# Optimization experiments

Measured on AMD Instinct MI355X. Metric: run time of the kernel, lower is better.

The kernel has to match this reference:

```python
import jax, jax.numpy as jnp
import numpy as np

B, C, Z, H, W = 1, 64, 8, 32, 32
C8 = C // 8


def setup_inputs() -> dict:
    key = jax.random.key(0)
    ks = jax.random.split(key, 8)
    shp = (B, C, Z, H, W)
    return {
        "x1": jax.random.normal(ks[0], shp, dtype=jnp.float32),
        "x2": jax.random.normal(ks[1], shp, dtype=jnp.float32),
        # 1x1x1 Conv3d weights are pointwise channel matmuls: [out, in]
        "Wf": jax.random.normal(ks[2], (C8, C), dtype=jnp.float32) * (1.0 / np.sqrt(C)),
        "bf": jnp.zeros((C8,), dtype=jnp.float32),
        "Wg": jax.random.normal(ks[3], (C8, C), dtype=jnp.float32) * (1.0 / np.sqrt(C)),
        "bg": jnp.zeros((C8,), dtype=jnp.float32),
        "Wh1": jax.random.normal(ks[4], (C, C), dtype=jnp.float32) * (1.0 / np.sqrt(C)),
        "bh1": jnp.zeros((C,), dtype=jnp.float32),
        "Wh2": jax.random.normal(ks[5], (C, C), dtype=jnp.float32) * (1.0 / np.sqrt(C)),
        "bh2": jnp.zeros((C,), dtype=jnp.float32),
        "gamma1": jax.random.uniform(ks[6], (1,), dtype=jnp.float32),
        "gamma2": jax.random.uniform(ks[7], (1,), dtype=jnp.float32),
    }


def _attend(x, Wf, bf, Wg, bg, Wh, bh, gamma):
    b, c, z, h, w = x.shape
    n = z * h * w
    xf = x.reshape(b, c, n)                                  # [B, C, N]
    f = jnp.einsum('oc,bcn->bno', Wf, xf) + bf               # [B, N, C//8]
    g = jnp.einsum('oc,bcn->bon', Wg, xf) + bg[:, None]      # [B, C//8, N]
    # unscaled attention logits, softmax over last dim (torch dim=2)
    att = jax.nn.softmax(jnp.einsum('bnk,bkm->bnm', f, g), axis=2)  # [B, N, N]
    v = jnp.einsum('oc,bcn->bon', Wh, xf) + bh[:, None]      # [B, C, N]
    sa = jnp.einsum('bcn,bnm->bcm', v, att).reshape(x.shape)  # h @ attention
    return gamma * sa + x


def reference(x1, x2, Wf, bf, Wg, bg, Wh1, bh1, Wh2, bh2, gamma1, gamma2):
    y1 = _attend(x1, Wf, bf, Wg, bg, Wh1, bh1, gamma1)
    y2 = _attend(x2, Wf, bf, Wg, bg, Wh2, bh2, gamma2)
    return (y1, y2)
```

## Files before the change

kernel.cpp:

```cpp
#include <hip/hip_runtime.h>
#include <math.h>

#define N 8192
#define WSP (80*N)
#define OFF_G (8*N)
#define OFF_T (16*N)

typedef __attribute__((ext_vector_type(8)))  short bf16x8;
typedef __attribute__((ext_vector_type(4)))  float f32x4;
typedef __attribute__((ext_vector_type(16))) float f32x16;

#define ZERO16 ((f32x16){0.f,0.f,0.f,0.f,0.f,0.f,0.f,0.f,0.f,0.f,0.f,0.f,0.f,0.f,0.f,0.f})

#if defined(__has_builtin)
#  if __has_builtin(__builtin_amdgcn_exp2f)
#    define EXP2(x) __builtin_amdgcn_exp2f(x)
#  endif
#endif
#ifndef EXP2
#  define EXP2(x) exp2f(x)
#endif

__device__ __forceinline__ unsigned short bf_hi(float x) {
    union { float f; unsigned u; } v; v.f = x;
    unsigned r = v.u + 0x7fffu + ((v.u >> 16) & 1u);
    return (unsigned short)(r >> 16);
}
__device__ __forceinline__ float bf_f(unsigned short h) {
    union { float f; unsigned u; } v; v.u = ((unsigned)h) << 16;
    return v.f;
}
__device__ __forceinline__ unsigned pack_hi16(unsigned i1, unsigned i0) {
#if defined(__has_builtin) && __has_builtin(__builtin_amdgcn_perm)
    return __builtin_amdgcn_perm(i1, i0, 0x07060302u);
#else
    return (i1 & 0xffff0000u) | (i0 >> 16);
#endif
}

__device__ __forceinline__ void xcd_map(int lin, int& a, int& idx) {
    int xcd = lin & 7;
    a   = xcd >> 2;
    idx = (xcd & 3) | ((lin >> 3) << 2);
}

__global__ __launch_bounds__(512) void prep_kernel(
    const float* __restrict__ x1, const float* __restrict__ x2,
    const float* __restrict__ Wf, const float* __restrict__ bf,
    const float* __restrict__ Wg, const float* __restrict__ bg,
    const float* __restrict__ Wh1, const float* __restrict__ bh1,
    const float* __restrict__ Wh2, const float* __restrict__ bh2,
    float* __restrict__ ws)
{
    int a, bidx;
    xcd_map(blockIdx.x + (int)gridDim.x * blockIdx.y, a, bidx);
    const float* x  = a ? x2  : x1;
    const float* Wh = a ? Wh2 : Wh1;
    const float* bh = a ? bh2 : bh1;
    float* base = ws + (size_t)a * WSP;
    unsigned short* F16 = (unsigned short*)base;
    unsigned short* G16 = (unsigned short*)(base + OFF_G);
    float* vb = base + OFF_T;

    __shared__ __align__(16) float xs[32][68];
    __shared__ __align__(16) float Wlds[80][64];
    __shared__ float blds[80];

    const int n0 = bidx * 32;
    const int t  = threadIdx.x;
    for (int i = t; i < 64*32; i += 512) {
        int c = i >> 5, j = i & 31;
        xs[j][c] = x[(size_t)c*N + n0 + j];
    }
    for (int i4 = t; i4 < 80*16; i4 += 512) {
        int o = i4 >> 4, c4 = i4 & 15;
        const float* src = (o < 8) ? (Wf + o*64) : (o < 16) ? (Wg + (o-8)*64) : (Wh + (o-16)*64);
        *(f32x4*)&Wlds[o][c4*4] = *(const f32x4*)(src + c4*4);
    }
    if (t < 80) blds[t] = (t < 8) ? bf[t] : (t < 16) ? bg[t-8] : bh[t-16];
    __syncthreads();

    const int j  = t & 31;
    const int og = t >> 5;
    float s[5];
    #pragma unroll
    for (int k = 0; k < 5; ++k) s[k] = blds[og + 16*k];
    const f32x4* xrow = (const f32x4*)&xs[j][0];
    #pragma unroll 4
    for (int c4 = 0; c4 < 16; ++c4) {
        const f32x4 xv = xrow[c4];
        #pragma unroll
        for (int k = 0; k < 5; ++k) {
            const f32x4 wv = *(const f32x4*)&Wlds[og + 16*k][c4*4];
            s[k] += wv.x * xv.x;
            s[k] += wv.y * xv.y;
            s[k] += wv.z * xv.z;
            s[k] += wv.w * xv.w;
        }
    }
    const float LOG2E = 1.44269504088896340736f;
    #pragma unroll
    for (int k = 0; k < 5; ++k) {
        int o = og + 16*k;
        if (o < 8) {
            float v = s[k] * LOG2E;
            unsigned short h = bf_hi(v);
            F16[(size_t)(n0+j)*16 + o]     = h;
            F16[(size_t)(n0+j)*16 + 8 + o] = bf_hi(v - bf_f(h));
        } else if (o < 16) {
            float v = s[k];
            unsigned short h = bf_hi(v);
            G16[(size_t)(n0+j)*16 + (o-8)]     = h;
            G16[(size_t)(n0+j)*16 + 8 + (o-8)] = bf_hi(v - bf_f(h));
        } else {
            vb[(size_t)(o-16)*N + n0 + j] = s[k];
        }
    }
}

__global__ __launch_bounds__(512, 4) void rownorm_kernel(float* __restrict__ ws)
{
    int a, bidx;
    xcd_map(blockIdx.x + (int)gridDim.x * blockIdx.y, a, bidx);
    float* base = ws + (size_t)a * WSP;
    const unsigned short* F16 = (const unsigned short*)base;
    const unsigned short* G16 = (const unsigned short*)(base + OFF_G);
    float* vb = base + OFF_T;
    const int n0 = bidx * 32;
    const int t  = threadIdx.x;
    const int w = t >> 6, lane = t & 63, l31 = lane & 31, hi = lane >> 5;

    __shared__ float vbs[32][65];
    __shared__ float lsum[8][32];
    __shared__ float linv[32];

    {
        const int c = t >> 3, g = t & 7;
        const f32x4 v = __builtin_nontemporal_load(
            (const f32x4*)(vb + (size_t)c*N + n0 + g*4));
        vbs[g*4+0][c] = v.x;
        vbs[g*4+1][c] = v.y;
        vbs[g*4+2][c] = v.z;
        vbs[g*4+3][c] = v.w;
    }

    const bf16x8 A1 = *(const bf16x8*)(F16 + (size_t)(n0 + l31)*16 + hi*8);
    const bf16x8 z8 = {0,0,0,0,0,0,0,0};
    const bf16x8 A2 = hi ? z8 : A1;

    const int mb = w * (N/8);
    const int MM = (N/8) - 1;
    bf16x8 B1, B2;
    f32x16 S, sum = ZERO16;

    B1 = *(const bf16x8*)(G16 + (size_t)(mb + l31)*16);
    B2 = *(const bf16x8*)(G16 + (size_t)(mb + l31)*16 + 8);
    S = __builtin_amdgcn_mfma_f32_32x32x16_bf16(A1, B1, ZERO16, 0, 0, 0);
    S = __builtin_amdgcn_mfma_f32_32x32x16_bf16(A2, B2, S, 0, 0, 0);
    B1 = *(const bf16x8*)(G16 + (size_t)(mb + 32 + l31)*16);
    B2 = *(const bf16x8*)(G16 + (size_t)(mb + 32 + l31)*16 + 8);

    for (int it = 0; it < 32; ++it) {
        f32x16 Sn = __builtin_amdgcn_mfma_f32_32x32x16_bf16(A1, B1, ZERO16, 0, 0, 0);
        Sn = __builtin_amdgcn_mfma_f32_32x32x16_bf16(A2, B2, Sn, 0, 0, 0);
        {
            const size_t mrow = mb + (((it+2)*32) & MM) + l31;
            B1 = *(const bf16x8*)(G16 + mrow*16);
            B2 = *(const bf16x8*)(G16 + mrow*16 + 8);
        }
        #pragma unroll
        for (int r = 0; r < 16; ++r)
            sum[r] += __uint_as_float(__float_as_uint(EXP2(S[r])) & 0xffff0000u);
        S = Sn;
    }
    #pragma unroll
    for (int r = 0; r < 16; ++r) {
        float v = sum[r];
        v += __shfl_xor(v, 1, 64);
        v += __shfl_xor(v, 2, 64);
        v += __shfl_xor(v, 4, 64);
        v += __shfl_xor(v, 8, 64);
        v += __shfl_xor(v, 16, 64);
        sum[r] = v;
    }
    if (l31 == 0) {
        #pragma unroll
        for (int r = 0; r < 16; ++r) {
            int n = (r & 3) + 8*(r >> 2) + 4*hi;
            lsum[w][n] = sum[r];
        }
    }
    __syncthreads();
    if (t < 32) {
        float v = 0.f;
        #pragma unroll
        for (int ww = 0; ww < 8; ++ww) v += lsum[ww][t];
        linv[t] = 1.0f / v;
    }
    __syncthreads();

    if (t < 256) {
        const int c = t >> 2, kkg = t & 3;
        bf16x8 H;
        #pragma unroll
        for (int jj = 0; jj < 8; ++jj) {
            int n_rd = (kkg >> 1)*16 + 4*(kkg & 1) + (jj & 3) + 8*((jj >> 2) & 1);
            H[jj] = (short)bf_hi(vbs[n_rd][c] * linv[n_rd]);
        }
        unsigned short* tile = (unsigned short*)(base + OFF_T) + (size_t)(n0 >> 5) * 4096;
        *(bf16x8*)(tile + c*32 + kkg*8) = H;
    }
}

__global__ __launch_bounds__(768, 3) void attn_kernel(
    const float* __restrict__ x1, const float* __restrict__ x2,
    const float* __restrict__ ga1, const float* __restrict__ ga2,
    const float* __restrict__ ws, float* __restrict__ out_)
{
    int a, bidx;
    xcd_map(blockIdx.x + (int)gridDim.x * blockIdx.y, a, bidx);
    const float* x = a ? x2 : x1;
    const float gamma = a ? ga2[0] : ga1[0];
    const float* base = ws + (size_t)a * WSP;
    const unsigned short* F16 = (const unsigned short*)base;
    const unsigned short* G16 = (const unsigned short*)(base + OFF_G);
    const unsigned short* tiles = (const unsigned short*)(base + OFF_T);
    float* out = out_ + (size_t)a * ((size_t)64 * N);

    const int m0 = bidx * 64;
    const int t = threadIdx.x;
    const int w = t >> 6, lane = t & 63, l31 = lane & 31, hi = lane >> 5;

    const bf16x8 z8 = {0,0,0,0,0,0,0,0};
    bf16x8 Bh0, Bl0, Bh1, Bl1;
    {
        const unsigned short* gp0 = G16 + (size_t)(m0 + l31)*16;
        const unsigned short* gp1 = G16 + (size_t)(m0 + 32 + l31)*16;
        Bh0 = *(const bf16x8*)gp0;
        Bl0 = hi ? z8 : *(const bf16x8*)(gp0 + 8);
        Bh1 = *(const bf16x8*)gp1;
        Bl1 = hi ? z8 : *(const bf16x8*)(gp1 + 8);
    }

    f32x16 accA = ZERO16, accB = ZERO16;
    f32x16 accC = ZERO16, accD = ZERO16;

    const int beg = 21*w + (w < 4 ? w : 4);
    const int end = beg + (w < 4 ? 22 : 21);

    bf16x8 Acur, Anxt;
    bf16x8 AH[4];

    Acur = *(const bf16x8*)(F16 + ((size_t)beg*32 + l31)*16 + hi*8);
    Anxt = *(const bf16x8*)(F16 + ((size_t)(beg+1)*32 + l31)*16 + hi*8);
    {
        const unsigned short* tb = tiles + (size_t)beg * 4096;
        #pragma unroll
        for (int kp = 0; kp < 2; ++kp)
            #pragma unroll
            for (int ct = 0; ct < 2; ++ct)
                AH[kp*2+ct] = *(const bf16x8*)(tb + (ct*32 + l31)*32 + kp*16 + hi*8);
    }

    for (int it = beg; it < end; ++it) {
        int in1 = it + 1; if (in1 >= end) in1 -= (end - beg);
        int in2 = it + 2; if (in2 >= end) in2 -= (end - beg);

        f32x16 S0 = __builtin_amdgcn_mfma_f32_32x32x16_bf16(Acur, Bh0, ZERO16, 0, 0, 0);
        f32x16 S1 = __builtin_amdgcn_mfma_f32_32x32x16_bf16(Acur, Bh1, ZERO16, 0, 0, 0);
        S0 = __builtin_amdgcn_mfma_f32_32x32x16_bf16(Acur, Bl0, S0, 0, 0, 0);
        S1 = __builtin_amdgcn_mfma_f32_32x32x16_bf16(Acur, Bl1, S1, 0, 0, 0);
        Acur = Anxt;
        Anxt = *(const bf16x8*)(F16 + ((size_t)in2*32 + l31)*16 + hi*8);

        union BU { bf16x8 v; unsigned u[4]; };
        BU pH0[2], pH1[2];
        #pragma unroll
        for (int kp = 0; kp < 2; ++kp)
            #pragma unroll
            for (int d = 0; d < 4; ++d) {
                float q0 = EXP2(S0[kp*8 + 2*d]);
                float q1 = EXP2(S0[kp*8 + 2*d + 1]);
                pH0[kp].u[d] = pack_hi16(__float_as_uint(q1), __float_as_uint(q0));
                float q2 = EXP2(S1[kp*8 + 2*d]);
                float q3 = EXP2(S1[kp*8 + 2*d + 1]);
                pH1[kp].u[d] = pack_hi16(__float_as_uint(q3), __float_as_uint(q2));
            }

        #pragma unroll
        for (int kp = 0; kp < 2; ++kp) {
            accA = __builtin_amdgcn_mfma_f32_32x32x16_bf16(AH[kp*2+0], pH0[kp].v, accA, 0, 0, 0);
            accC = __builtin_amdgcn_mfma_f32_32x32x16_bf16(AH[kp*2+0], pH1[kp].v, accC, 0, 0, 0);
            accB = __builtin_amdgcn_mfma_f32_32x32x16_bf16(AH[kp*2+1], pH0[kp].v, accB, 0, 0, 0);
            accD = __builtin_amdgcn_mfma_f32_32x32x16_bf16(AH[kp*2+1], pH1[kp].v, accD, 0, 0, 0);
        }

        {
            const unsigned short* tb = tiles + (size_t)in1 * 4096;
            #pragma unroll
            for (int kp = 0; kp < 2; ++kp)
                #pragma unroll
                for (int ct = 0; ct < 2; ++ct)
                    AH[kp*2+ct] = *(const bf16x8*)(tb + (ct*32 + l31)*32 + kp*16 + hi*8);
        }
    }

    __shared__ float red[64][65];
    for (int ww = 0; ww < 12; ++ww) {
        if (w == ww) {
            #pragma unroll
            for (int mg = 0; mg < 2; ++mg)
                #pragma unroll
                for (int ct = 0; ct < 2; ++ct) {
                    const f32x16& Ac = mg ? (ct ? accD : accC) : (ct ? accB : accA);
                    #pragma unroll
                    for (int r = 0; r < 16; ++r) {
                        int c = ct*32 + (r & 3) + 8*(r >> 2) + 4*hi;
                        int m = mg*32 + l31;
                        if (ww == 0) red[c][m]  = Ac[r];
                        else         red[c][m] += Ac[r];
                    }
                }
        }
        __syncthreads();
    }
    for (int e = t; e < 64*64; e += 768) {
        int c = e >> 6, m = e & 63;
        size_t gi = (size_t)c*N + m0 + m;
        float xv = __builtin_nontemporal_load(x + gi);
        __builtin_nontemporal_store(gamma * red[c][m] + xv, out + gi);
    }
}

extern "C" void kernel_launch(void* const* d_in, const int* in_sizes, int n_in,
                              void* d_out, int out_size, void* d_ws, size_t ws_size,
                              hipStream_t stream)
{
    (void)in_sizes; (void)n_in; (void)out_size; (void)ws_size;
    const float* x1  = (const float*)d_in[0];
    const float* x2  = (const float*)d_in[1];
    const float* Wf  = (const float*)d_in[2];
    const float* bf  = (const float*)d_in[3];
    const float* Wg  = (const float*)d_in[4];
    const float* bg  = (const float*)d_in[5];
    const float* Wh1 = (const float*)d_in[6];
    const float* bh1 = (const float*)d_in[7];
    const float* Wh2 = (const float*)d_in[8];
    const float* bh2 = (const float*)d_in[9];
    const float* g1  = (const float*)d_in[10];
    const float* g2  = (const float*)d_in[11];
    float* out = (float*)d_out;
    float* ws  = (float*)d_ws;

    prep_kernel   <<<dim3(N/32, 2), dim3(512), 0, stream>>>(x1,x2,Wf,bf,Wg,bg,Wh1,bh1,Wh2,bh2,ws);
    rownorm_kernel<<<dim3(N/32, 2), dim3(512), 0, stream>>>(ws);
    attn_kernel   <<<dim3(N/64, 2), dim3(768), 0, stream>>>(x1,x2,g1,g2,ws,out);
}
```

Measured before the change: 141.4 us.

## Software-pipeline logits MFMA one iteration ahead of exp and PV MFMAs

Restructures the inner attention loop so the logit MFMAs for the next tile are issued while exp2 and pack run on the current tile. The PV MFMAs are split into two halves interleaved with the exp work. The aim is to hide MFMA latency behind VALU transcendental work instead of stalling on S0/S1 each iteration. It adds a prologue and keeps S0/S1 live across iterations, which raises register pressure.

Result: no change. 139.5 us (-1.3%).

```diff
diff --git a/kernel.cpp b/kernel.cpp
--- a/kernel.cpp
+++ b/kernel.cpp
@@ -248,11 +248,18 @@
     const int beg = 21*w + (w < 4 ? w : 4);
     const int end = beg + (w < 4 ? 22 : 21);
 
-    bf16x8 Acur, Anxt;
+    bf16x8 Acur;
     bf16x8 AH[4];
-
-    Acur = *(const bf16x8*)(F16 + ((size_t)beg*32 + l31)*16 + hi*8);
-    Anxt = *(const bf16x8*)(F16 + ((size_t)(beg+1)*32 + l31)*16 + hi*8);
+    f32x16 S0, S1;
+
+    {
+        const bf16x8 A0 = *(const bf16x8*)(F16 + ((size_t)beg*32 + l31)*16 + hi*8);
+        S0 = __builtin_amdgcn_mfma_f32_32x32x16_bf16(A0, Bh0, ZERO16, 0, 0, 0);
+        S1 = __builtin_amdgcn_mfma_f32_32x32x16_bf16(A0, Bh1, ZERO16, 0, 0, 0);
+        S0 = __builtin_amdgcn_mfma_f32_32x32x16_bf16(A0, Bl0, S0, 0, 0, 0);
+        S1 = __builtin_amdgcn_mfma_f32_32x32x16_bf16(A0, Bl1, S1, 0, 0, 0);
+    }
+    Acur = *(const bf16x8*)(F16 + ((size_t)(beg+1)*32 + l31)*16 + hi*8);
     {
         const unsigned short* tb = tiles + (size_t)beg * 4096;
         #pragma unroll
@@ -262,38 +269,48 @@
                 AH[kp*2+ct] = *(const bf16x8*)(tb + (ct*32 + l31)*32 + kp*16 + hi*8);
     }
 
+    union BU { bf16x8 v; unsigned u[4]; };
+
     for (int it = beg; it < end; ++it) {
         int in1 = it + 1; if (in1 >= end) in1 -= (end - beg);
         int in2 = it + 2; if (in2 >= end) in2 -= (end - beg);
 
-        f32x16 S0 = __builtin_amdgcn_mfma_f32_32x32x16_bf16(Acur, Bh0, ZERO16, 0, 0, 0);
-        f32x16 S1 = __builtin_amdgcn_mfma_f32_32x32x16_bf16(Acur, Bh1, ZERO16, 0, 0, 0);
+        BU pH0a, pH1a;
+        #pragma unroll
+        for (int d = 0; d < 4; ++d) {
+            float q0 = EXP2(S0[2*d]);
+            float q1 = EXP2(S0[2*d + 1]);
+            pH0a.u[d] = pack_hi16(__float_as_uint(q1), __float_as_uint(q0));
+            float q2 = EXP2(S1[2*d]);
+            float q3 = EXP2(S1[2*d + 1]);
+            pH1a.u[d] = pack_hi16(__float_as_uint(q3), __float_as_uint(q2));
+        }
+        accA = __builtin_amdgcn_mfma_f32_32x32x16_bf16(AH[0], pH0a.v, accA, 0, 0, 0);
+        accC = __builtin_amdgcn_mfma_f32_32x32x16_bf16(AH[0], pH1a.v, accC, 0, 0, 0);
+        accB = __builtin_amdgcn_mfma_f32_32x32x16_bf16(AH[1], pH0a.v, accB, 0, 0, 0);
+        accD = __builtin_amdgcn_mfma_f32_32x32x16_bf16(AH[1], pH1a.v, accD, 0, 0, 0);
+
+        BU pH0b, pH1b;
+        #pragma unroll
+        for (int d = 0; d < 4; ++d) {
+            float q0 = EXP2(S0[8 + 2*d]);
+            float q1 = EXP2(S0[8 + 2*d + 1]);
+            pH0b.u[d] = pack_hi16(__float_as_uint(q1), __float_as_uint(q0));
+            float q2 = EXP2(S1[8 + 2*d]);
+            float q3 = EXP2(S1[8 + 2*d + 1]);
+            pH1b.u[d] = pack_hi16(__float_as_uint(q3), __float_as_uint(q2));
+        }
+
+        S0 = __builtin_amdgcn_mfma_f32_32x32x16_bf16(Acur, Bh0, ZERO16, 0, 0, 0);
+        S1 = __builtin_amdgcn_mfma_f32_32x32x16_bf16(Acur, Bh1, ZERO16, 0, 0, 0);
         S0 = __builtin_amdgcn_mfma_f32_32x32x16_bf16(Acur, Bl0, S0, 0, 0, 0);
         S1 = __builtin_amdgcn_mfma_f32_32x32x16_bf16(Acur, Bl1, S1, 0, 0, 0);
-        Acur = Anxt;
-        Anxt = *(const bf16x8*)(F16 + ((size_t)in2*32 + l31)*16 + hi*8);
-
-        union BU { bf16x8 v; unsigned u[4]; };
-        BU pH0[2], pH1[2];
-        #pragma unroll
-        for (int kp = 0; kp < 2; ++kp)
-            #pragma unroll
-            for (int d = 0; d < 4; ++d) {
-                float q0 = EXP2(S0[kp*8 + 2*d]);
-                float q1 = EXP2(S0[kp*8 + 2*d + 1]);
-                pH0[kp].u[d] = pack_hi16(__float_as_uint(q1), __float_as_uint(q0));
-                float q2 = EXP2(S1[kp*8 + 2*d]);
-                float q3 = EXP2(S1[kp*8 + 2*d + 1]);
-                pH1[kp].u[d] = pack_hi16(__float_as_uint(q3), __float_as_uint(q2));
-            }
-
-        #pragma unroll
-        for (int kp = 0; kp < 2; ++kp) {
-            accA = __builtin_amdgcn_mfma_f32_32x32x16_bf16(AH[kp*2+0], pH0[kp].v, accA, 0, 0, 0);
-            accC = __builtin_amdgcn_mfma_f32_32x32x16_bf16(AH[kp*2+0], pH1[kp].v, accC, 0, 0, 0);
-            accB = __builtin_amdgcn_mfma_f32_32x32x16_bf16(AH[kp*2+1], pH0[kp].v, accB, 0, 0, 0);
-            accD = __builtin_amdgcn_mfma_f32_32x32x16_bf16(AH[kp*2+1], pH1[kp].v, accD, 0, 0, 0);
-        }
+        Acur = *(const bf16x8*)(F16 + ((size_t)in2*32 + l31)*16 + hi*8);
+
+        accA = __builtin_amdgcn_mfma_f32_32x32x16_bf16(AH[2], pH0b.v, accA, 0, 0, 0);
+        accC = __builtin_amdgcn_mfma_f32_32x32x16_bf16(AH[2], pH1b.v, accC, 0, 0, 0);
+        accB = __builtin_amdgcn_mfma_f32_32x32x16_bf16(AH[3], pH0b.v, accB, 0, 0, 0);
+        accD = __builtin_amdgcn_mfma_f32_32x32x16_bf16(AH[3], pH1b.v, accD, 0, 0, 0);
 
         {
             const unsigned short* tb = tiles + (size_t)in1 * 4096;
```

## Use 8 waves with 32 tiles each and a two-stage software pipeline

Applied to the files above, without the earlier changes.

The attention kernel drops from 12 to 8 wavefronts per block, and each wave now owns exactly 32 key tiles instead of an uneven 21/22 split. The main loop is restructured to handle two tiles per iteration: the logits MFMAs for the next pair are issued after the PV MFMAs of the current pair, and tile and A-operand loads are prefetched one stage ahead. This aims to hide exp/pack latency and memory latency behind MFMA work and to shorten the cross-wave shared-memory reduction. In exchange it raises register pressure and gives fewer waves per CU (launch bounds 512,2), which can reduce latency hiding.

Measured after the change: 148.2 us. 4.9% more time.

```diff
diff --git a/kernel.cpp b/kernel.cpp
--- a/kernel.cpp
+++ b/kernel.cpp
@@ -212,7 +212,50 @@
     }
 }
 
-__global__ __launch_bounds__(768, 3) void attn_kernel(
+#define MFMA_(A_, B_, C_) __builtin_amdgcn_mfma_f32_32x32x16_bf16(A_, B_, C_, 0, 0, 0)
+
+#define PACK_QUAD(P0_, P1_, S0_, S1_, O_)                                      \
+    _Pragma("unroll")                                                          \
+    for (int d = 0; d < 4; ++d) {                                              \
+        float q0 = EXP2(S0_[(O_) + 2*d]), q1 = EXP2(S0_[(O_) + 2*d + 1]);      \
+        P0_.u[d] = pack_hi16(__float_as_uint(q1), __float_as_uint(q0));        \
+        float q2 = EXP2(S1_[(O_) + 2*d]), q3 = EXP2(S1_[(O_) + 2*d + 1]);      \
+        P1_.u[d] = pack_hi16(__float_as_uint(q3), __float_as_uint(q2));        \
+    }
+
+#define CHUNK_PV(S0_, S1_, T0_, T1_, T2_, T3_)                                 \
+    {                                                                          \
+        BU u0_, u1_;                                                           \
+        PACK_QUAD(u0_, u1_, S0_, S1_, 0)                                       \
+        accA = MFMA_(T0_, u0_.v, accA);                                        \
+        accC = MFMA_(T0_, u1_.v, accC);                                        \
+        accB = MFMA_(T1_, u0_.v, accB);                                        \
+        accD = MFMA_(T1_, u1_.v, accD);                                        \
+        BU v0_, v1_;                                                           \
+        PACK_QUAD(v0_, v1_, S0_, S1_, 8)                                       \
+        accA = MFMA_(T2_, v0_.v, accA);                                        \
+        accC = MFMA_(T2_, v1_.v, accC);                                        \
+        accB = MFMA_(T3_, v0_.v, accB);                                        \
+        accD = MFMA_(T3_, v1_.v, accD);                                        \
+    }
+
+#define LOAD_TILES(T0_, T1_, T2_, T3_, REL_)                                   \
+    {                                                                          \
+        const unsigned short* tb_ = tiles + (size_t)(cb + ((REL_) & 31)) * 4096; \
+        T0_ = *(const bf16x8*)(tb_ + (0*32 + l31)*32 + 0*16 + hi*8);           \
+        T1_ = *(const bf16x8*)(tb_ + (1*32 + l31)*32 + 0*16 + hi*8);           \
+        T2_ = *(const bf16x8*)(tb_ + (0*32 + l31)*32 + 1*16 + hi*8);           \
+        T3_ = *(const bf16x8*)(tb_ + (1*32 + l31)*32 + 1*16 + hi*8);           \
+    }
+
+#define LOAD_A(DST_, REL_)                                                     \
+    DST_ = *(const bf16x8*)(F16 + (size_t)((cb + ((REL_) & 31))*32 + l31)*16 + hi*8);
+
+#define LOGITS(S0_, S1_, A_)                                                   \
+    S0_ = MFMA_(A_, Bh0, ZERO16); S1_ = MFMA_(A_, Bh1, ZERO16);                \
+    S0_ = MFMA_(A_, Bl0, S0_);    S1_ = MFMA_(A_, Bl1, S1_);
+
+__global__ __launch_bounds__(512, 2) void attn_kernel(
     const float* __restrict__ x1, const float* __restrict__ x2,
     const float* __restrict__ ga1, const float* __restrict__ ga2,
     const float* __restrict__ ws, float* __restrict__ out_)
@@ -245,68 +288,39 @@
     f32x16 accA = ZERO16, accB = ZERO16;
     f32x16 accC = ZERO16, accD = ZERO16;
 
-    const int beg = 21*w + (w < 4 ? w : 4);
-    const int end = beg + (w < 4 ? 22 : 21);
-
-    bf16x8 Acur, Anxt;
-    bf16x8 AH[4];
-
-    Acur = *(const bf16x8*)(F16 + ((size_t)beg*32 + l31)*16 + hi*8);
-    Anxt = *(const bf16x8*)(F16 + ((size_t)(beg+1)*32 + l31)*16 + hi*8);
+    const int cb = w * 32;
+
+    union BU { bf16x8 v; unsigned u[4]; };
+
+    bf16x8 Aa, Ab;
+    bf16x8 AHa0, AHa1, AHa2, AHa3;
+    bf16x8 AHb0, AHb1, AHb2, AHb3;
+    f32x16 Sa0, Sa1, Sb0, Sb1;
+
     {
-        const unsigned short* tb = tiles + (size_t)beg * 4096;
-        #pragma unroll
-        for (int kp = 0; kp < 2; ++kp)
-            #pragma unroll
-            for (int ct = 0; ct < 2; ++ct)
-                AH[kp*2+ct] = *(const bf16x8*)(tb + (ct*32 + l31)*32 + kp*16 + hi*8);
-    }
-
-    for (int it = beg; it < end; ++it) {
-        int in1 = it + 1; if (in1 >= end) in1 -= (end - beg);
-        int in2 = it + 2; if (in2 >= end) in2 -= (end - beg);
-
-        f32x16 S0 = __builtin_amdgcn_mfma_f32_32x32x16_bf16(Acur, Bh0, ZERO16, 0, 0, 0);
-        f32x16 S1 = __builtin_amdgcn_mfma_f32_32x32x16_bf16(Acur, Bh1, ZERO16, 0, 0, 0);
-        S0 = __builtin_amdgcn_mfma_f32_32x32x16_bf16(Acur, Bl0, S0, 0, 0, 0);
-        S1 = __builtin_amdgcn_mfma_f32_32x32x16_bf16(Acur, Bl1, S1, 0, 0, 0);
-        Acur = Anxt;
-        Anxt = *(const bf16x8*)(F16 + ((size_t)in2*32 + l31)*16 + hi*8);
-
-        union BU { bf16x8 v; unsigned u[4]; };
-        BU pH0[2], pH1[2];
-        #pragma unroll
-        for (int kp = 0; kp < 2; ++kp)
-            #pragma unroll
-            for (int d = 0; d < 4; ++d) {
-                float q0 = EXP2(S0[kp*8 + 2*d]);
-                float q1 = EXP2(S0[kp*8 + 2*d + 1]);
-                pH0[kp].u[d] = pack_hi16(__float_as_uint(q1), __float_as_uint(q0));
-                float q2 = EXP2(S1[kp*8 + 2*d]);
-                float q3 = EXP2(S1[kp*8 + 2*d + 1]);
-                pH1[kp].u[d] = pack_hi16(__float_as_uint(q3), __float_as_uint(q2));
-            }
-
-        #pragma unroll
-        for (int kp = 0; kp < 2; ++kp) {
-            accA = __builtin_amdgcn_mfma_f32_32x32x16_bf16(AH[kp*2+0], pH0[kp].v, accA, 0, 0, 0);
-            accC = __builtin_amdgcn_mfma_f32_32x32x16_bf16(AH[kp*2+0], pH1[kp].v, accC, 0, 0, 0);
-            accB = __builtin_amdgcn_mfma_f32_32x32x16_bf16(AH[kp*2+1], pH0[kp].v, accB, 0, 0, 0);
-            accD = __builtin_amdgcn_mfma_f32_32x32x16_bf16(AH[kp*2+1], pH1[kp].v, accD, 0, 0, 0);
-        }
-
-        {
-            const unsigned short* tb = tiles + (size_t)in1 * 4096;
-            #pragma unroll
-            for (int kp = 0; kp < 2; ++kp)
-                #pragma unroll
-                for (int ct = 0; ct < 2; ++ct)
-                    AH[kp*2+ct] = *(const bf16x8*)(tb + (ct*32 + l31)*32 + kp*16 + hi*8);
-        }
+        bf16x8 A0; LOAD_A(A0, 0)
+        LOGITS(Sa0, Sa1, A0)
+        bf16x8 A1v; LOAD_A(A1v, 1)
+        LOGITS(Sb0, Sb1, A1v)
+    }
+    LOAD_TILES(AHa0, AHa1, AHa2, AHa3, 0)
+    LOAD_TILES(AHb0, AHb1, AHb2, AHb3, 1)
+    LOAD_A(Aa, 2)
+    LOAD_A(Ab, 3)
+
+    for (int it = 0; it < 16; ++it) {
+        CHUNK_PV(Sa0, Sa1, AHa0, AHa1, AHa2, AHa3)
+        LOAD_TILES(AHa0, AHa1, AHa2, AHa3, 2*it + 2)
+        CHUNK_PV(Sb0, Sb1, AHb0, AHb1, AHb2, AHb3)
+        LOAD_TILES(AHb0, AHb1, AHb2, AHb3, 2*it + 3)
+        LOGITS(Sa0, Sa1, Aa)
+        LOGITS(Sb0, Sb1, Ab)
+        LOAD_A(Aa, 2*it + 4)
+        LOAD_A(Ab, 2*it + 5)
     }
 
     __shared__ float red[64][65];
-    for (int ww = 0; ww < 12; ++ww) {
+    for (int ww = 0; ww < 8; ++ww) {
         if (w == ww) {
             #pragma unroll
             for (int mg = 0; mg < 2; ++mg)
@@ -324,7 +338,9 @@
         }
         __syncthreads();
     }
-    for (int e = t; e < 64*64; e += 768) {
+    #pragma unroll
+    for (int i = 0; i < 8; ++i) {
+        int e = t + 512*i;
         int c = e >> 6, m = e & 63;
         size_t gi = (size_t)c*N + m0 + m;
         float xv = __builtin_nontemporal_load(x + gi);
@@ -354,5 +370,5 @@
 
     prep_kernel   <<<dim3(N/32, 2), dim3(512), 0, stream>>>(x1,x2,Wf,bf,Wg,bg,Wh1,bh1,Wh2,bh2,ws);
     rownorm_kernel<<<dim3(N/32, 2), dim3(512), 0, stream>>>(ws);
-    attn_kernel   <<<dim3(N/64, 2), dim3(768), 0, stream>>>(x1,x2,g1,g2,ws,out);
-}
+    attn_kernel   <<<dim3(N/64, 2), dim3(512), 0, stream>>>(x1,x2,g1,g2,ws,out);
+}
```
